# Kernel optimization log

Hardware: AMD Instinct MI355X
Metric: run time of the kernel (lower is better)

Reference implementation:

```python
import jax, jax.numpy as jnp
import numpy as np

DIM = 1024
N_EXPERTS = 8
TOP_K = 2
EXPERT_HIDDEN = DIM * 2
B, T = 4, 4096


def setup_inputs() -> dict:
    key = jax.random.key(0)
    ks = jax.random.split(key, 5)
    # xavier_uniform with gain=0.02 for w1/w2 (fan_in=DIM, fan_out=EXPERT_HIDDEN)
    lim12 = 0.02 * np.sqrt(6.0 / (DIM + EXPERT_HIDDEN))
    lim3 = 0.02 * np.sqrt(6.0 / (EXPERT_HIDDEN + DIM))
    x = jax.random.normal(ks[0], (B, T, DIM), dtype=jnp.float32)
    router_w = 0.02 * jax.random.normal(ks[1], (N_EXPERTS, DIM), dtype=jnp.float32)
    w1 = jax.random.uniform(ks[2], (N_EXPERTS, DIM, EXPERT_HIDDEN), minval=-lim12, maxval=lim12, dtype=jnp.float32)
    w2 = jax.random.uniform(ks[3], (N_EXPERTS, DIM, EXPERT_HIDDEN), minval=-lim12, maxval=lim12, dtype=jnp.float32)
    w3 = jax.random.uniform(ks[4], (N_EXPERTS, EXPERT_HIDDEN, DIM), minval=-lim3, maxval=lim3, dtype=jnp.float32)
    return {"x": x, "router_w": router_w, "w1": w1, "w2": w2, "w3": w3}


def reference(x, router_w, w1, w2, w3):
    # Router: top-k softmax gating, renormalized over the selected k.
    logits = jnp.einsum('btd,ed->bte', x, router_w)          # [B,T,E]
    probs = jax.nn.softmax(logits, axis=-1)
    topk_vals, topk_idx = jax.lax.top_k(probs, TOP_K)        # [B,T,K]
    topk_weights = topk_vals / topk_vals.sum(axis=-1, keepdims=True)

    out = jnp.zeros_like(x)
    for e in range(N_EXPERTS):
        # gate weight for expert e per token (0 if e not in token's top-k)
        w_e = jnp.where(topk_idx == e, topk_weights, 0.0).sum(axis=-1)  # [B,T]
        h = jax.nn.silu(jnp.einsum('btd,dh->bth', x, w1[e])) * jnp.einsum('btd,dh->bth', x, w2[e])
        out = out + jnp.einsum('bth,hd->btd', h, w3[e]) * w_e[..., None]
    aux_loss = jnp.float32(0.0)  # eval mode
    return (out, aux_loss)
```

## Files before the change

kernel.cpp:

```cpp
#include <hip/hip_runtime.h>
#include <stdint.h>

#define TTOK 16384
#define NDIM 1024
#define NHID 2048
#define NEXP 8
#define TM 256
#define MAXT 136
#define SLOTCAP (2 * TTOK + NEXP * TM)

typedef __attribute__((ext_vector_type(8))) short short8;
typedef __attribute__((ext_vector_type(4))) float f32x4;

__device__ __forceinline__ unsigned short f2bf(float f) {
  unsigned int u = __float_as_uint(f);
  u += 0x7FFFu + ((u >> 16) & 1u);
  return (unsigned short)(u >> 16);
}

__device__ __forceinline__ void gload16(const void* g, void* l) {
  __builtin_amdgcn_global_load_lds(
      (const __attribute__((address_space(1))) unsigned int*)g,
      (__attribute__((address_space(3))) unsigned int*)l, 16, 0, 0);
}

__device__ __forceinline__ float silu(float z) {
  return z / (1.0f + __expf(-z));
}

__device__ __forceinline__ void router_block(int b, const float* __restrict__ x,
                                             const float* __restrict__ rw,
                                             unsigned short* __restrict__ xbf,
                                             int* __restrict__ tok_e,
                                             float* __restrict__ tok_gw) {
  int t = (b << 2) + (threadIdx.x >> 6);
  int lane = threadIdx.x & 63;
  const float4* xr = (const float4*)(x + (size_t)t * NDIM);

  float4 v[4];
  float d[NEXP];
#pragma unroll
  for (int e = 0; e < NEXP; ++e) d[e] = 0.f;

#pragma unroll
  for (int i = 0; i < 4; ++i) {
    int c = i * 64 + lane;
    v[i] = xr[c];
#pragma unroll
    for (int e = 0; e < NEXP; ++e) {
      float4 w = ((const float4*)(rw + e * NDIM))[c];
      d[e] += v[i].x * w.x + v[i].y * w.y + v[i].z * w.z + v[i].w * w.w;
    }
  }
#pragma unroll
  for (int e = 0; e < NEXP; ++e)
    for (int s = 32; s; s >>= 1) d[e] += __shfl_xor(d[e], s, 64);

  unsigned short* xo = xbf + (size_t)t * NDIM;
#pragma unroll
  for (int i = 0; i < 4; ++i) {
    int c = i * 64 + lane;
    ushort4 u;
    u.x = f2bf(v[i].x); u.y = f2bf(v[i].y); u.z = f2bf(v[i].z); u.w = f2bf(v[i].w);
    ((ushort4*)xo)[c] = u;
  }

  if (lane == 0) {
    float m = d[0];
#pragma unroll
    for (int e = 1; e < NEXP; ++e) m = fmaxf(m, d[e]);
    float ex[NEXP];
#pragma unroll
    for (int e = 0; e < NEXP; ++e) ex[e] = __expf(d[e] - m);
    int e0 = 0;
#pragma unroll
    for (int e = 1; e < NEXP; ++e) if (ex[e] > ex[e0]) e0 = e;
    int e1 = (e0 == 0) ? 1 : 0;
#pragma unroll
    for (int e = 0; e < NEXP; ++e) if (e != e0 && ex[e] > ex[e1]) e1 = e;
    float p0 = ex[e0], p1 = ex[e1];
    float inv = 1.f / (p0 + p1);
    tok_e[2 * t] = e0; tok_e[2 * t + 1] = e1;
    tok_gw[2 * t] = p0 * inv; tok_gw[2 * t + 1] = p1 * inv;
  }
}

__device__ __forceinline__ void tconv_tile(const float* __restrict__ src,
                                           unsigned short* __restrict__ dst,
                                           int R, int C, int bx, int by) {
  __shared__ unsigned short tile[64][65];
  int tx = threadIdx.x & 15, ty = threadIdx.x >> 4;
#pragma unroll
  for (int rr = 0; rr < 4; ++rr) {
    int rl = rr * 16 + ty;
    float4 v = *(const float4*)(src + (size_t)(by + rl) * C + bx + tx * 4);
    tile[rl][tx * 4 + 0] = f2bf(v.x);
    tile[rl][tx * 4 + 1] = f2bf(v.y);
    tile[rl][tx * 4 + 2] = f2bf(v.z);
    tile[rl][tx * 4 + 3] = f2bf(v.w);
  }
  __syncthreads();
#pragma unroll
  for (int rr = 0; rr < 4; ++rr) {
    int cl = rr * 16 + ty;
    ushort4 u;
    u.x = tile[tx * 4 + 0][cl];
    u.y = tile[tx * 4 + 1][cl];
    u.z = tile[tx * 4 + 2][cl];
    u.w = tile[tx * 4 + 3][cl];
    *(ushort4*)(dst + (size_t)(bx + cl) * R + by + tx * 4) = u;
  }
}

__global__ void k_prep(const float* __restrict__ x, const float* __restrict__ rw,
                       unsigned short* __restrict__ xbf, int* __restrict__ tok_e,
                       float* __restrict__ tok_gw, const float* __restrict__ w1,
                       const float* __restrict__ w2, const float* __restrict__ w3,
                       unsigned short* __restrict__ w1t, unsigned short* __restrict__ w2t,
                       unsigned short* __restrict__ w3t) {
  int b = blockIdx.x;
  if (b < 4096) {
    router_block(b, x, rw, xbf, tok_e, tok_gw);
    return;
  }
  int tcb = b - 4096;
  int bx = tcb & 31;
  int by = (tcb >> 5) & 15;
  int z = tcb >> 9;
  if (z < 16) {
    int e = z & 7;
    const float* src = (z < 8 ? w1 : w2) + (size_t)e * NDIM * NHID;
    unsigned short* dst = (z < 8 ? w1t : w2t) + (size_t)e * NDIM * NHID;
    tconv_tile(src, dst, NDIM, NHID, bx * 64, by * 64);
  } else {
    int e = z - 16;
    const float* src = w3 + (size_t)e * NHID * NDIM;
    unsigned short* dst = w3t + (size_t)e * NHID * NDIM;
    tconv_tile(src, dst, NHID, NDIM, by * 64, bx * 64);
  }
}

__global__ void k_count(const int* __restrict__ tok_e, unsigned int* __restrict__ counts) {
  __shared__ unsigned int h[NEXP];
  int tid = threadIdx.x;
  if (tid < NEXP) h[tid] = 0u;
  __syncthreads();
  for (int i = blockIdx.x * 256 + tid; i < 2 * TTOK; i += gridDim.x * 256)
    atomicAdd(&h[tok_e[i]], 1u);
  __syncthreads();
  if (tid < NEXP) atomicAdd(&counts[tid], h[tid]);
}

__global__ void k_offsets(const unsigned int* __restrict__ counts,
                          unsigned int* __restrict__ slotbase, unsigned int* __restrict__ cnt2,
                          unsigned int* __restrict__ tile_e, unsigned int* __restrict__ tile_m0) {
  int l = threadIdx.x;
  unsigned int c[NEXP], base[NEXP], tb[NEXP];
  unsigned int b = 0, t = 0;
#pragma unroll
  for (int e = 0; e < NEXP; ++e) {
    c[e] = counts[e];
    base[e] = b; tb[e] = t;
    unsigned int nt = (c[e] + TM - 1) / TM;
    b += nt * TM; t += nt;
  }
  if (l < NEXP) { slotbase[l] = base[l]; cnt2[l] = 0u; }
  for (int idx = l; idx < MAXT; idx += 64) {
    unsigned int te = 0xFFFFFFFFu, tm = 0;
#pragma unroll
    for (int e = 0; e < NEXP; ++e) {
      unsigned int nt = (c[e] + TM - 1) / TM;
      if ((unsigned)idx >= tb[e] && (unsigned)idx < tb[e] + nt) {
        te = (unsigned)e; tm = base[e] + ((unsigned)idx - tb[e]) * TM;
      }
    }
    tile_e[idx] = te; tile_m0[idx] = tm;
  }
}

__global__ void k_fill(const int* __restrict__ tok_e, const float* __restrict__ tok_gw,
                       const unsigned int* __restrict__ slotbase, unsigned int* __restrict__ cnt2,
                       unsigned int* __restrict__ tok_list, float* __restrict__ gate_list) {
  __shared__ unsigned int hcnt[NEXP];
  __shared__ unsigned int hbase[NEXP];
  int tid = threadIdx.x;
  int t = blockIdx.x * 256 + tid;
  if (tid < NEXP) hcnt[tid] = 0u;
  __syncthreads();
  int e0 = tok_e[2 * t], e1 = tok_e[2 * t + 1];
  float g0 = tok_gw[2 * t], g1 = tok_gw[2 * t + 1];
  unsigned int p0 = atomicAdd(&hcnt[e0], 1u);
  unsigned int p1 = atomicAdd(&hcnt[e1], 1u);
  __syncthreads();
  if (tid < NEXP) hbase[tid] = atomicAdd(&cnt2[tid], hcnt[tid]);
  __syncthreads();
  unsigned int s0 = slotbase[e0] + hbase[e0] + p0;
  unsigned int s1 = slotbase[e1] + hbase[e1] + p1;
  tok_list[s0] = (unsigned)t; gate_list[s0] = g0;
  tok_list[s1] = (unsigned)t; gate_list[s1] = g1;
}

__global__ void k_sentinel(float* __restrict__ out, float v) {
  if (threadIdx.x == 0 && blockIdx.x == 0) out[0] = v;
}

__global__ __launch_bounds__(512, 2) void k_gemm12(
    const unsigned short* __restrict__ xbf, const unsigned short* __restrict__ w1t,
    const unsigned short* __restrict__ w2t, unsigned short* __restrict__ H,
    const unsigned int* __restrict__ tok_list, const unsigned int* __restrict__ tile_e,
    const unsigned int* __restrict__ tile_m0) {
  unsigned int e = tile_e[blockIdx.y];
  if (e > 7u) return;
  int m0 = (int)tile_m0[blockIdx.y];
  int n0 = blockIdx.x * 128;

  __shared__ unsigned short As[256 * 64];
  __shared__ unsigned short B1s[128 * 64];
  __shared__ unsigned short B2s[128 * 64];

  int tid = threadIdx.x, w = tid >> 6, l = tid & 63;
  int rsub = tid >> 3;
  int swb = ((tid & 7) * 16) ^ ((rsub & 7) << 4);

  const unsigned short* aS[4];
#pragma unroll
  for (int jj = 0; jj < 4; ++jj) {
    int row = jj * 64 + rsub;
    aS[jj] = xbf + (size_t)tok_list[m0 + row] * NDIM + (swb >> 1);
  }
  const unsigned short* b1S[2];
  const unsigned short* b2S[2];
#pragma unroll
  for (int jj = 0; jj < 2; ++jj) {
    int row = jj * 64 + rsub;
    size_t off = ((size_t)e * NHID + n0 + row) * NDIM + (swb >> 1);
    b1S[jj] = w1t + off;
    b2S[jj] = w2t + off;
  }
  int ldsb = w * 1024;

  f32x4 acc1[8][2], acc2[8][2];
#pragma unroll
  for (int m = 0; m < 8; ++m)
#pragma unroll
    for (int n = 0; n < 2; ++n) { acc1[m][n] = (f32x4)0.f; acc2[m][n] = (f32x4)0.f; }

  int wr = (w >> 2) * 128, wc = (w & 3) * 32;

  short8 ar[8], b1r[4], b2r[4];

  auto rdA_mh0_B1 = [&]() {
#pragma unroll
    for (int ks = 0; ks < 2; ++ks) {
      int kb = ks * 64 + ((l >> 4) << 4);
#pragma unroll
      for (int m = 0; m < 4; ++m) {
        int r = wr + m * 16 + (l & 15);
        ar[ks * 4 + m] = *(const short8*)((const char*)As + r * 128 + (kb ^ ((r & 7) << 4)));
      }
#pragma unroll
      for (int n = 0; n < 2; ++n) {
        int r = wc + n * 16 + (l & 15);
        b1r[ks * 2 + n] = *(const short8*)((const char*)B1s + r * 128 + (kb ^ ((r & 7) << 4)));
      }
    }
  };
  auto rdB2 = [&]() {
#pragma unroll
    for (int ks = 0; ks < 2; ++ks) {
      int kb = ks * 64 + ((l >> 4) << 4);
#pragma unroll
      for (int n = 0; n < 2; ++n) {
        int r = wc + n * 16 + (l & 15);
        b2r[ks * 2 + n] = *(const short8*)((const char*)B2s + r * 128 + (kb ^ ((r & 7) << 4)));
      }
    }
  };
  auto rdA_mh1 = [&]() {
#pragma unroll
    for (int ks = 0; ks < 2; ++ks) {
      int kb = ks * 64 + ((l >> 4) << 4);
#pragma unroll
      for (int m = 0; m < 4; ++m) {
        int r = wr + 64 + m * 16 + (l & 15);
        ar[ks * 4 + m] = *(const short8*)((const char*)As + r * 128 + (kb ^ ((r & 7) << 4)));
      }
    }
  };
  auto mfma1 = [&](int mh) {
    __builtin_amdgcn_s_setprio(1);
#pragma unroll
    for (int ks = 0; ks < 2; ++ks)
#pragma unroll
      for (int m = 0; m < 4; ++m)
#pragma unroll
        for (int n = 0; n < 2; ++n)
          acc1[mh * 4 + m][n] = __builtin_amdgcn_mfma_f32_16x16x32_bf16(
              ar[ks * 4 + m], b1r[ks * 2 + n], acc1[mh * 4 + m][n], 0, 0, 0);
    __builtin_amdgcn_s_setprio(0);
  };
  auto mfma2 = [&](int mh) {
    __builtin_amdgcn_s_setprio(1);
#pragma unroll
    for (int ks = 0; ks < 2; ++ks)
#pragma unroll
      for (int m = 0; m < 4; ++m)
#pragma unroll
        for (int n = 0; n < 2; ++n)
          acc2[mh * 4 + m][n] = __builtin_amdgcn_mfma_f32_16x16x32_bf16(
              ar[ks * 4 + m], b2r[ks * 2 + n], acc2[mh * 4 + m][n], 0, 0, 0);
    __builtin_amdgcn_s_setprio(0);
  };

  for (int t = 0; t < 16; ++t) {
    int ke = t * 64;
#pragma unroll
    for (int jj = 0; jj < 4; ++jj)
      gload16(aS[jj] + ke, (char*)As + jj * 8192 + ldsb);
#pragma unroll
    for (int jj = 0; jj < 2; ++jj) {
      gload16(b1S[jj] + ke, (char*)B1s + jj * 8192 + ldsb);
      gload16(b2S[jj] + ke, (char*)B2s + jj * 8192 + ldsb);
    }
    asm volatile("s_waitcnt vmcnt(0)" ::: "memory");
    __builtin_amdgcn_s_barrier();

    rdA_mh0_B1();
    mfma1(0);
    rdB2();
    mfma2(0);
    rdA_mh1();
    mfma1(1);
    mfma2(1);

    __builtin_amdgcn_s_barrier();
  }

#pragma unroll
  for (int m = 0; m < 8; ++m)
#pragma unroll
    for (int n = 0; n < 2; ++n) {
      int col = n0 + wc + n * 16 + (l & 15);
#pragma unroll
      for (int q = 0; q < 4; ++q) {
        int slot = m0 + wr + m * 16 + ((l >> 4) << 2) + q;
        float hv = silu(acc1[m][n][q]) * acc2[m][n][q];
        H[(size_t)slot * NHID + col] = f2bf(hv);
      }
    }
}

__global__ __launch_bounds__(256, 2) void k_gemm3(
    const unsigned short* __restrict__ H, const unsigned short* __restrict__ w3t,
    float* __restrict__ out, const unsigned int* __restrict__ tok_list,
    const float* __restrict__ gate_list, const unsigned int* __restrict__ tile_e,
    const unsigned int* __restrict__ tile_m0) {
  unsigned int e = tile_e[blockIdx.y >> 1];
  if (e > 7u) return;
  int m0 = (int)tile_m0[blockIdx.y >> 1] + (int)(blockIdx.y & 1) * 128;
  int n0 = blockIdx.x * 128;

  __shared__ unsigned short As[128 * 64];
  __shared__ unsigned short Bs[128 * 64];

  int tid = threadIdx.x, w = tid >> 6, l = tid & 63;
  int rsub = tid >> 3;
  int swb = ((tid & 7) * 16) ^ ((rsub & 7) << 4);

  const unsigned short* aS[4];
  const unsigned short* bS[4];
#pragma unroll
  for (int jj = 0; jj < 4; ++jj) {
    int row = jj * 32 + rsub;
    aS[jj] = H + (size_t)(m0 + row) * NHID + (swb >> 1);
    bS[jj] = w3t + ((size_t)e * NDIM + n0 + row) * NHID + (swb >> 1);
  }
  int ldsb = w * 1024;

  f32x4 acc[4][4];
#pragma unroll
  for (int m = 0; m < 4; ++m)
#pragma unroll
    for (int n = 0; n < 4; ++n) acc[m][n] = (f32x4)0.f;

  int wr = (w >> 1) * 64, wc = (w & 1) * 64;

  for (int t = 0; t < 32; ++t) {
    int ke = t * 64;
#pragma unroll
    for (int jj = 0; jj < 4; ++jj) {
      gload16(aS[jj] + ke, (char*)As + jj * 4096 + ldsb);
      gload16(bS[jj] + ke, (char*)Bs + jj * 4096 + ldsb);
    }
    __syncthreads();
#pragma unroll
    for (int ks = 0; ks < 2; ++ks) {
      int kb = ks * 64 + ((l >> 4) << 4);
      short8 a[4], b[4];
#pragma unroll
      for (int m = 0; m < 4; ++m) {
        int r = wr + m * 16 + (l & 15);
        a[m] = *(const short8*)((const char*)As + r * 128 + (kb ^ ((r & 7) << 4)));
      }
#pragma unroll
      for (int n = 0; n < 4; ++n) {
        int r = wc + n * 16 + (l & 15);
        b[n] = *(const short8*)((const char*)Bs + r * 128 + (kb ^ ((r & 7) << 4)));
      }
#pragma unroll
      for (int m = 0; m < 4; ++m)
#pragma unroll
        for (int n = 0; n < 4; ++n)
          acc[m][n] = __builtin_amdgcn_mfma_f32_16x16x32_bf16(a[m], b[n], acc[m][n], 0, 0, 0);
    }
    __syncthreads();
  }

#pragma unroll
  for (int m = 0; m < 4; ++m)
#pragma unroll
    for (int q = 0; q < 4; ++q) {
      int slot = m0 + wr + m * 16 + ((l >> 4) << 2) + q;
      unsigned int tok = tok_list[slot];
      float g = gate_list[slot];
      if (g != 0.f) {
        float* orow = out + (size_t)tok * NDIM + n0 + wc;
#pragma unroll
        for (int n = 0; n < 4; ++n)
          atomicAdd(orow + n * 16 + (l & 15), acc[m][n][q] * g);
      }
    }
}

extern "C" void kernel_launch(void* const* d_in, const int* in_sizes, int n_in,
                              void* d_out, int out_size, void* d_ws, size_t ws_size,
                              hipStream_t stream) {
  const float* x = (const float*)d_in[0];
  const float* rw = (const float*)d_in[1];
  const float* w1 = (const float*)d_in[2];
  const float* w2 = (const float*)d_in[3];
  const float* w3 = (const float*)d_in[4];
  float* out = (float*)d_out;
  char* ws = (char*)d_ws;

  size_t o = 0;
  auto alloc = [&](size_t b) { size_t r = o; o = (o + b + 255) & ~(size_t)255; return r; };
  size_t o_xbf = alloc((size_t)TTOK * NDIM * 2);
  size_t o_w3t = alloc((size_t)NEXP * NDIM * NHID * 2);
  size_t o_H = alloc((size_t)SLOTCAP * NHID * 2);
  size_t o_tok = alloc((size_t)SLOTCAP * 4);
  size_t o_gate = alloc((size_t)SLOTCAP * 4);
  size_t o_te = alloc((size_t)TTOK * 2 * 4);
  size_t o_tg = alloc((size_t)TTOK * 2 * 4);
  size_t o_cnt = alloc(64);
  size_t o_cnt2 = alloc(64);
  size_t o_sb = alloc(64);
  size_t o_tle = alloc(MAXT * 4 + 64);
  size_t o_tlm = alloc(MAXT * 4 + 64);
  size_t need = o;

  size_t outBytes = (size_t)out_size * sizeof(float);
  size_t wtBytes = (size_t)NEXP * NDIM * NHID * 2;

  if (ws_size < need || outBytes < 2 * wtBytes) {
    hipMemsetAsync(d_out, 0, outBytes, stream);
    k_sentinel<<<1, 64, 0, stream>>>(out, (float)((double)ws_size / 1048576.0));
    return;
  }

  unsigned short* xbf = (unsigned short*)(ws + o_xbf);
  unsigned short* w3t = (unsigned short*)(ws + o_w3t);
  unsigned short* Hbuf = (unsigned short*)(ws + o_H);
  unsigned int* tok_list = (unsigned int*)(ws + o_tok);
  float* gate_list = (float*)(ws + o_gate);
  int* tok_e = (int*)(ws + o_te);
  float* tok_gw = (float*)(ws + o_tg);
  unsigned int* counts = (unsigned int*)(ws + o_cnt);
  unsigned int* cnt2 = (unsigned int*)(ws + o_cnt2);
  unsigned int* slotbase = (unsigned int*)(ws + o_sb);
  unsigned int* tile_e = (unsigned int*)(ws + o_tle);
  unsigned int* tile_m0 = (unsigned int*)(ws + o_tlm);

  unsigned short* w1t = (unsigned short*)d_out;
  unsigned short* w2t = (unsigned short*)((char*)d_out + wtBytes);

  hipMemsetAsync(counts, 0, 64, stream);
  hipMemsetAsync(tok_list, 0, (size_t)SLOTCAP * 4, stream);
  hipMemsetAsync(gate_list, 0, (size_t)SLOTCAP * 4, stream);

  k_prep<<<16384, 256, 0, stream>>>(x, rw, xbf, tok_e, tok_gw, w1, w2, w3, w1t, w2t, w3t);
  k_count<<<64, 256, 0, stream>>>(tok_e, counts);
  k_offsets<<<1, 64, 0, stream>>>(counts, slotbase, cnt2, tile_e, tile_m0);
  k_fill<<<TTOK / 256, 256, 0, stream>>>(tok_e, tok_gw, slotbase, cnt2, tok_list, gate_list);

  k_gemm12<<<dim3(NHID / 128, MAXT), 512, 0, stream>>>(xbf, w1t, w2t, Hbuf, tok_list,
                                                       tile_e, tile_m0);

  hipMemsetAsync(d_out, 0, outBytes, stream);

  k_gemm3<<<dim3(NDIM / 128, 2 * MAXT), 256, 0, stream>>>(Hbuf, w3t, out, tok_list, gate_list,
                                                          tile_e, tile_m0);
}
```

Before: 720.0 us.

## Interleave w1/w2 rows and double-buffer LDS in gate-up GEMM

Weight prep now writes w1 and w2 interleaved in groups of 16 rows into one combined B matrix, so the gate-up GEMM treats them as a single 256-wide B tile with unified accumulators. The main loop gains double-buffered LDS with staged global-to-LDS loads spread across the compute phases and partial vmcnt waits, so loads for the next K step overlap the MFMAs. LDS use doubles to 128 KB per block, which may cut occupancy below the requested two blocks per CU. The more complex barrier schedule also risks races.

```diff
diff --git a/kernel.cpp b/kernel.cpp
--- a/kernel.cpp
+++ b/kernel.cpp
@@ -87,7 +87,7 @@
 
 __device__ __forceinline__ void tconv_tile(const float* __restrict__ src,
                                            unsigned short* __restrict__ dst,
-                                           int R, int C, int bx, int by) {
+                                           int R, int C, int bx, int by, int mode) {
   __shared__ unsigned short tile[64][65];
   int tx = threadIdx.x & 15, ty = threadIdx.x >> 4;
 #pragma unroll
@@ -108,7 +108,11 @@
     u.y = tile[tx * 4 + 1][cl];
     u.z = tile[tx * 4 + 2][cl];
     u.w = tile[tx * 4 + 3][cl];
-    *(ushort4*)(dst + (size_t)(bx + cl) * R + by + tx * 4) = u;
+    int c = bx + cl;
+    size_t row;
+    if (mode == 0) row = (size_t)c;
+    else row = (size_t)(32 * (c >> 4) + (c & 15) + (mode == 2 ? 16 : 0));
+    *(ushort4*)(dst + row * R + by + tx * 4) = u;
   }
 }
 
@@ -116,8 +120,7 @@
                        unsigned short* __restrict__ xbf, int* __restrict__ tok_e,
                        float* __restrict__ tok_gw, const float* __restrict__ w1,
                        const float* __restrict__ w2, const float* __restrict__ w3,
-                       unsigned short* __restrict__ w1t, unsigned short* __restrict__ w2t,
-                       unsigned short* __restrict__ w3t) {
+                       unsigned short* __restrict__ wBt, unsigned short* __restrict__ w3t) {
   int b = blockIdx.x;
   if (b < 4096) {
     router_block(b, x, rw, xbf, tok_e, tok_gw);
@@ -130,13 +133,13 @@
   if (z < 16) {
     int e = z & 7;
     const float* src = (z < 8 ? w1 : w2) + (size_t)e * NDIM * NHID;
-    unsigned short* dst = (z < 8 ? w1t : w2t) + (size_t)e * NDIM * NHID;
-    tconv_tile(src, dst, NDIM, NHID, bx * 64, by * 64);
+    unsigned short* dst = wBt + (size_t)e * 2 * NHID * NDIM;
+    tconv_tile(src, dst, NDIM, NHID, bx * 64, by * 64, z < 8 ? 1 : 2);
   } else {
     int e = z - 16;
     const float* src = w3 + (size_t)e * NHID * NDIM;
     unsigned short* dst = w3t + (size_t)e * NHID * NDIM;
-    tconv_tile(src, dst, NHID, NDIM, by * 64, bx * 64);
+    tconv_tile(src, dst, NHID, NDIM, by * 64, bx * 64, 0);
   }
 }
 
@@ -205,89 +208,84 @@
 }
 
 __global__ __launch_bounds__(512, 2) void k_gemm12(
-    const unsigned short* __restrict__ xbf, const unsigned short* __restrict__ w1t,
-    const unsigned short* __restrict__ w2t, unsigned short* __restrict__ H,
-    const unsigned int* __restrict__ tok_list, const unsigned int* __restrict__ tile_e,
-    const unsigned int* __restrict__ tile_m0) {
+    const unsigned short* __restrict__ xbf, const unsigned short* __restrict__ wBt,
+    unsigned short* __restrict__ H, const unsigned int* __restrict__ tok_list,
+    const unsigned int* __restrict__ tile_e, const unsigned int* __restrict__ tile_m0) {
   unsigned int e = tile_e[blockIdx.y];
   if (e > 7u) return;
   int m0 = (int)tile_m0[blockIdx.y];
-  int n0 = blockIdx.x * 128;
-
-  __shared__ unsigned short As[256 * 64];
-  __shared__ unsigned short B1s[128 * 64];
-  __shared__ unsigned short B2s[128 * 64];
+  int n0c = blockIdx.x * 256;
+
+  __shared__ unsigned short As[2][256 * 64];
+  __shared__ unsigned short Bs[2][256 * 64];
 
   int tid = threadIdx.x, w = tid >> 6, l = tid & 63;
   int rsub = tid >> 3;
   int swb = ((tid & 7) * 16) ^ ((rsub & 7) << 4);
 
-  const unsigned short* aS[4];
-#pragma unroll
-  for (int jj = 0; jj < 4; ++jj) {
-    int row = jj * 64 + rsub;
-    aS[jj] = xbf + (size_t)tok_list[m0 + row] * NDIM + (swb >> 1);
-  }
-  const unsigned short* b1S[2];
-  const unsigned short* b2S[2];
-#pragma unroll
-  for (int jj = 0; jj < 2; ++jj) {
-    int row = jj * 64 + rsub;
-    size_t off = ((size_t)e * NHID + n0 + row) * NDIM + (swb >> 1);
-    b1S[jj] = w1t + off;
-    b2S[jj] = w2t + off;
-  }
-  int ldsb = w * 1024;
-
-  f32x4 acc1[8][2], acc2[8][2];
+  const unsigned short* aP[2][2];
+#pragma unroll
+  for (int g = 0; g < 2; ++g)
+#pragma unroll
+    for (int c = 0; c < 2; ++c) {
+      int r = 64 * g + 128 * c + rsub;
+      aP[g][c] = xbf + (size_t)tok_list[m0 + r] * NDIM + (swb >> 1);
+    }
+  const unsigned short* bP[2][2];
+  size_t ebase = (size_t)e * 2 * NHID * NDIM;
+#pragma unroll
+  for (int g = 0; g < 2; ++g)
+#pragma unroll
+    for (int c = 0; c < 2; ++c) {
+      int r = 32 * g + 128 * c + (rsub & 31) + 64 * (rsub >> 5);
+      bP[g][c] = wBt + ebase + (size_t)(n0c + r) * NDIM + (swb >> 1);
+    }
+  int aD0 = w * 1024;
+  int bD0 = (w & 3) * 1024 + 8192 * (w >> 2);
+
+  f32x4 acc[8][4];
 #pragma unroll
   for (int m = 0; m < 8; ++m)
 #pragma unroll
-    for (int n = 0; n < 2; ++n) { acc1[m][n] = (f32x4)0.f; acc2[m][n] = (f32x4)0.f; }
-
-  int wr = (w >> 2) * 128, wc = (w & 3) * 32;
-
-  short8 ar[8], b1r[4], b2r[4];
-
-  auto rdA_mh0_B1 = [&]() {
+    for (int n = 0; n < 4; ++n) acc[m][n] = (f32x4)0.f;
+
+  int wr = (w >> 2) * 128, wc = (w & 3) * 64;
+
+  short8 ar[8], br0[4], br1[4];
+
+  auto stageA = [&](int g, int kt, int buf) {
+#pragma unroll
+    for (int c = 0; c < 2; ++c)
+      gload16(aP[g][c] + kt * 64, (char*)As[buf] + 8192 * g + 16384 * c + aD0);
+  };
+  auto stageB = [&](int g, int kt, int buf) {
+#pragma unroll
+    for (int c = 0; c < 2; ++c)
+      gload16(bP[g][c] + kt * 64, (char*)Bs[buf] + 4096 * g + 16384 * c + bD0);
+  };
+  auto rdA = [&](const char* A, int mh) {
 #pragma unroll
     for (int ks = 0; ks < 2; ++ks) {
       int kb = ks * 64 + ((l >> 4) << 4);
 #pragma unroll
       for (int m = 0; m < 4; ++m) {
-        int r = wr + m * 16 + (l & 15);
-        ar[ks * 4 + m] = *(const short8*)((const char*)As + r * 128 + (kb ^ ((r & 7) << 4)));
-      }
-#pragma unroll
-      for (int n = 0; n < 2; ++n) {
-        int r = wc + n * 16 + (l & 15);
-        b1r[ks * 2 + n] = *(const short8*)((const char*)B1s + r * 128 + (kb ^ ((r & 7) << 4)));
+        int r = wr + mh * 64 + m * 16 + (l & 15);
+        ar[ks * 4 + m] = *(const short8*)(A + r * 128 + (kb ^ ((r & 7) << 4)));
       }
     }
   };
-  auto rdB2 = [&]() {
+  auto rdB = [&](const char* B, int nh, short8* br) {
 #pragma unroll
     for (int ks = 0; ks < 2; ++ks) {
       int kb = ks * 64 + ((l >> 4) << 4);
 #pragma unroll
       for (int n = 0; n < 2; ++n) {
-        int r = wc + n * 16 + (l & 15);
-        b2r[ks * 2 + n] = *(const short8*)((const char*)B2s + r * 128 + (kb ^ ((r & 7) << 4)));
+        int r = wc + nh * 32 + n * 16 + (l & 15);
+        br[ks * 2 + n] = *(const short8*)(B + r * 128 + (kb ^ ((r & 7) << 4)));
       }
     }
   };
-  auto rdA_mh1 = [&]() {
-#pragma unroll
-    for (int ks = 0; ks < 2; ++ks) {
-      int kb = ks * 64 + ((l >> 4) << 4);
-#pragma unroll
-      for (int m = 0; m < 4; ++m) {
-        int r = wr + 64 + m * 16 + (l & 15);
-        ar[ks * 4 + m] = *(const short8*)((const char*)As + r * 128 + (kb ^ ((r & 7) << 4)));
-      }
-    }
-  };
-  auto mfma1 = [&](int mh) {
+  auto quad = [&](int mh, int nh, const short8* br) {
     __builtin_amdgcn_s_setprio(1);
 #pragma unroll
     for (int ks = 0; ks < 2; ++ks)
@@ -295,57 +293,72 @@
       for (int m = 0; m < 4; ++m)
 #pragma unroll
         for (int n = 0; n < 2; ++n)
-          acc1[mh * 4 + m][n] = __builtin_amdgcn_mfma_f32_16x16x32_bf16(
-              ar[ks * 4 + m], b1r[ks * 2 + n], acc1[mh * 4 + m][n], 0, 0, 0);
+          acc[mh * 4 + m][nh * 2 + n] = __builtin_amdgcn_mfma_f32_16x16x32_bf16(
+              ar[ks * 4 + m], br[ks * 2 + n], acc[mh * 4 + m][nh * 2 + n], 0, 0, 0);
     __builtin_amdgcn_s_setprio(0);
   };
-  auto mfma2 = [&](int mh) {
-    __builtin_amdgcn_s_setprio(1);
-#pragma unroll
-    for (int ks = 0; ks < 2; ++ks)
-#pragma unroll
-      for (int m = 0; m < 4; ++m)
-#pragma unroll
-        for (int n = 0; n < 2; ++n)
-          acc2[mh * 4 + m][n] = __builtin_amdgcn_mfma_f32_16x16x32_bf16(
-              ar[ks * 4 + m], b2r[ks * 2 + n], acc2[mh * 4 + m][n], 0, 0, 0);
-    __builtin_amdgcn_s_setprio(0);
-  };
-
-  for (int t = 0; t < 16; ++t) {
-    int ke = t * 64;
-#pragma unroll
-    for (int jj = 0; jj < 4; ++jj)
-      gload16(aS[jj] + ke, (char*)As + jj * 8192 + ldsb);
-#pragma unroll
-    for (int jj = 0; jj < 2; ++jj) {
-      gload16(b1S[jj] + ke, (char*)B1s + jj * 8192 + ldsb);
-      gload16(b2S[jj] + ke, (char*)B2s + jj * 8192 + ldsb);
-    }
+
+  stageA(0, 0, 0);
+  stageB(0, 0, 0);
+  stageA(1, 0, 0);
+  stageB(1, 0, 0);
+
+  for (int t = 0; t < 15; ++t) {
+    int cur = t & 1, nb = cur ^ 1;
+    int ktN = t + 1;
+    const char* A = (const char*)As[cur];
+    const char* B = (const char*)Bs[cur];
+
+    stageA(0, ktN, nb);
+    asm volatile("s_waitcnt vmcnt(6)" ::: "memory");
+    __builtin_amdgcn_s_barrier();
+    rdA(A, 0);
+    rdB(B, 0, br0);
+    quad(0, 0, br0);
+    stageB(0, ktN, nb);
+    asm volatile("s_waitcnt vmcnt(4)" ::: "memory");
+    __builtin_amdgcn_s_barrier();
+    rdB(B, 1, br1);
+    quad(0, 1, br1);
+    stageA(1, ktN, nb);
+    __builtin_amdgcn_s_barrier();
+    rdA(A, 1);
+    quad(1, 1, br1);
+    stageB(1, ktN, nb);
+    __builtin_amdgcn_s_barrier();
+    quad(1, 0, br0);
+  }
+
+  {
+    const char* A = (const char*)As[1];
+    const char* B = (const char*)Bs[1];
+    asm volatile("s_waitcnt vmcnt(4)" ::: "memory");
+    __builtin_amdgcn_s_barrier();
+    rdA(A, 0);
+    rdB(B, 0, br0);
+    quad(0, 0, br0);
     asm volatile("s_waitcnt vmcnt(0)" ::: "memory");
     __builtin_amdgcn_s_barrier();
-
-    rdA_mh0_B1();
-    mfma1(0);
-    rdB2();
-    mfma2(0);
-    rdA_mh1();
-    mfma1(1);
-    mfma2(1);
-
-    __builtin_amdgcn_s_barrier();
-  }
-
+    rdB(B, 1, br1);
+    quad(0, 1, br1);
+    __builtin_amdgcn_s_barrier();
+    rdA(A, 1);
+    quad(1, 1, br1);
+    __builtin_amdgcn_s_barrier();
+    quad(1, 0, br0);
+  }
+
+  int gg0 = blockIdx.x * 8 + (w & 3) * 2;
 #pragma unroll
   for (int m = 0; m < 8; ++m)
 #pragma unroll
-    for (int n = 0; n < 2; ++n) {
-      int col = n0 + wc + n * 16 + (l & 15);
+    for (int nh = 0; nh < 2; ++nh) {
+      int hcol = (gg0 + nh) * 16 + (l & 15);
 #pragma unroll
       for (int q = 0; q < 4; ++q) {
         int slot = m0 + wr + m * 16 + ((l >> 4) << 2) + q;
-        float hv = silu(acc1[m][n][q]) * acc2[m][n][q];
-        H[(size_t)slot * NHID + col] = f2bf(hv);
+        float hv = silu(acc[m][nh * 2 + 0][q]) * acc[m][nh * 2 + 1][q];
+        H[(size_t)slot * NHID + hcol] = f2bf(hv);
       }
     }
 }
@@ -481,20 +494,19 @@
   unsigned int* tile_e = (unsigned int*)(ws + o_tle);
   unsigned int* tile_m0 = (unsigned int*)(ws + o_tlm);
 
-  unsigned short* w1t = (unsigned short*)d_out;
-  unsigned short* w2t = (unsigned short*)((char*)d_out + wtBytes);
+  unsigned short* wBt = (unsigned short*)d_out;
 
   hipMemsetAsync(counts, 0, 64, stream);
   hipMemsetAsync(tok_list, 0, (size_t)SLOTCAP * 4, stream);
   hipMemsetAsync(gate_list, 0, (size_t)SLOTCAP * 4, stream);
 
-  k_prep<<<16384, 256, 0, stream>>>(x, rw, xbf, tok_e, tok_gw, w1, w2, w3, w1t, w2t, w3t);
+  k_prep<<<16384, 256, 0, stream>>>(x, rw, xbf, tok_e, tok_gw, w1, w2, w3, wBt, w3t);
   k_count<<<64, 256, 0, stream>>>(tok_e, counts);
   k_offsets<<<1, 64, 0, stream>>>(counts, slotbase, cnt2, tile_e, tile_m0);
   k_fill<<<TTOK / 256, 256, 0, stream>>>(tok_e, tok_gw, slotbase, cnt2, tok_list, gate_list);
 
-  k_gemm12<<<dim3(NHID / 128, MAXT), 512, 0, stream>>>(xbf, w1t, w2t, Hbuf, tok_list,
-                                                       tile_e, tile_m0);
+  k_gemm12<<<dim3(2 * NHID / 256, MAXT), 512, 0, stream>>>(xbf, wBt, Hbuf, tok_list,
+                                                           tile_e, tile_m0);
 
   hipMemsetAsync(d_out, 0, outBytes, stream);
 
```

Measured after the change: 694.9 us. -3.5%, faster.
